# Performance work log

Hardware: AMD Instinct MI355X
Metric: run time of the kernel (lower is better)

Reference implementation:

```python
import jax, jax.numpy as jnp
import numpy as np

HIDDEN = 2048
HEAD_DIM = 128
GROUPS = 8
HEADS = HIDDEN // HEAD_DIM          # 16
HPG = HEADS // GROUPS               # heads per group = 2


def setup_inputs() -> dict:
    key = jax.random.key(0)
    ks = jax.random.split(key, 9)
    b, sl, sk = 2, 2048, 2048
    s = 0.02
    return {
        "q": jax.random.normal(ks[0], (b, sl, HIDDEN), jnp.float32),
        "k": jax.random.normal(ks[1], (b, sk, HIDDEN), jnp.float32),
        "v": jax.random.normal(ks[2], (b, sk, HIDDEN), jnp.float32),
        "Wq": jax.random.normal(ks[3], (HIDDEN, HIDDEN), jnp.float32) * s,
        "bq": jax.random.normal(ks[4], (HIDDEN,), jnp.float32) * s,
        "Wk": jax.random.normal(ks[5], (HIDDEN, HEAD_DIM * GROUPS), jnp.float32) * s,
        "bk": jax.random.normal(ks[6], (HEAD_DIM * GROUPS,), jnp.float32) * s,
        "Wv": jax.random.normal(ks[7], (HIDDEN, HEAD_DIM * GROUPS), jnp.float32) * s,
        "bv": jax.random.normal(ks[8], (HEAD_DIM * GROUPS,), jnp.float32) * s,
    }


def reference(q, k, v, Wq, bq, Wk, bk, Wv, bv):
    b, sl, _ = q.shape
    sk = k.shape[1]
    qp = q @ Wq + bq                                   # [b, sl, hidden]
    kp = k @ Wk + bk                                   # [b, sk, G*d]
    vp = v @ Wv + bv                                   # [b, sk, G*d]
    # head h = g*HPG + j uses group g, matching torch repeat_interleave on dim=1
    qh = qp.reshape(b, sl, GROUPS, HPG, HEAD_DIM).transpose(0, 2, 3, 1, 4)  # [b,G,hpg,sl,d]
    kh = kp.reshape(b, sk, GROUPS, HEAD_DIM).transpose(0, 2, 1, 3)          # [b,G,sk,d]
    vh = vp.reshape(b, sk, GROUPS, HEAD_DIM).transpose(0, 2, 1, 3)          # [b,G,sk,d]
    scale = 1.0 / jnp.sqrt(jnp.asarray(HEAD_DIM, qh.dtype))
    score = jnp.einsum("bghld,bgsd->bghls", qh, kh) * scale                 # [b,G,hpg,sl,sk]
    attn = jax.nn.softmax(score, axis=-1)
    out = jnp.einsum("bghls,bgsd->bghld", attn, vh)                         # [b,G,hpg,sl,d]
    out = out.transpose(0, 3, 1, 2, 4).reshape(b, sl, HIDDEN)
    return out
```

## Files before the change

kernel.cpp:

```cpp
#include <hip/hip_runtime.h>

typedef unsigned short u16;
typedef short v8s __attribute__((ext_vector_type(8)));
typedef float v4f __attribute__((ext_vector_type(4)));
typedef float v16f __attribute__((ext_vector_type(16)));

typedef __attribute__((address_space(3))) u16* lptr_t;
typedef const __attribute__((address_space(1))) void* gptr_t;

__device__ __forceinline__ u16 f2b(float f) {
  unsigned int u = __float_as_uint(f);
  u += 0x7fff + ((u >> 16) & 1);
  return (u16)(u >> 16);
}

__global__ __launch_bounds__(256) void prep_all(const float* __restrict__ q,
                                                const float* __restrict__ k,
                                                const float* __restrict__ v,
                                                const float* __restrict__ Wq,
                                                const float* __restrict__ Wk,
                                                const float* __restrict__ Wv,
                                                u16* __restrict__ qd,
                                                u16* __restrict__ kd,
                                                u16* __restrict__ vd,
                                                u16* __restrict__ wt) {
  __shared__ u16 tile[64][65];
  int blk = blockIdx.x;
  if (blk < 12288) {
    const float* s; u16* d;
    if (blk < 4096)      { s = q; d = qd; }
    else if (blk < 8192) { s = k; d = kd; blk -= 4096; }
    else                 { s = v; d = vd; blk -= 8192; }
    int i = (blk * 256 + threadIdx.x) * 8;
    float4 a = *(const float4*)&s[i];
    float4 b = *(const float4*)&s[i + 4];
    union { uint4 v4; u16 u[8]; } p;
    p.u[0] = f2b(a.x); p.u[1] = f2b(a.y); p.u[2] = f2b(a.z); p.u[3] = f2b(a.w);
    p.u[4] = f2b(b.x); p.u[5] = f2b(b.y); p.u[6] = f2b(b.z); p.u[7] = f2b(b.w);
    *(uint4*)&d[i] = p.v4;
    return;
  }
  blk -= 12288;
  const float* W; int N; u16* dst;
  if (blk < 1024)      { W = Wq; N = 2048; dst = wt; }
  else if (blk < 1536) { W = Wk; N = 1024; dst = wt + (size_t)2048 * 2048; blk -= 1024; }
  else                 { W = Wv; N = 1024; dst = wt + (size_t)3072 * 2048; blk -= 1536; }
  const int k0 = (blk & 31) * 64;
  const int n0 = (blk >> 5) * 64;
  const int t = threadIdx.x;
#pragma unroll
  for (int i = 0; i < 2; ++i) {
    int chunk = i * 256 + t;
    int kr = chunk >> 3;
    int nc = (chunk & 7) * 8;
    float4 a = *(const float4*)&W[(size_t)(k0 + kr) * N + n0 + nc];
    float4 b = *(const float4*)&W[(size_t)(k0 + kr) * N + n0 + nc + 4];
    tile[kr][nc + 0] = f2b(a.x); tile[kr][nc + 1] = f2b(a.y);
    tile[kr][nc + 2] = f2b(a.z); tile[kr][nc + 3] = f2b(a.w);
    tile[kr][nc + 4] = f2b(b.x); tile[kr][nc + 5] = f2b(b.y);
    tile[kr][nc + 6] = f2b(b.z); tile[kr][nc + 7] = f2b(b.w);
  }
  __syncthreads();
#pragma unroll
  for (int i = 0; i < 2; ++i) {
    int chunk = i * 256 + t;
    int nr = chunk >> 3;
    int kc = (chunk & 7) * 8;
    union { uint4 v; u16 u[8]; } cv;
#pragma unroll
    for (int j = 0; j < 8; ++j) cv.u[j] = tile[kc + j][nr];
    *(uint4*)&dst[(size_t)(n0 + nr) * 2048 + k0 + kc] = cv.v;
  }
}

__global__ __launch_bounds__(512, 2) void qkv_gemm8(const u16* __restrict__ qbf,
                                                    const u16* __restrict__ kbf,
                                                    const u16* __restrict__ vbf,
                                                    const u16* __restrict__ wt_all,
                                                    const float* __restrict__ bq,
                                                    const float* __restrict__ bk,
                                                    const float* __restrict__ bv,
                                                    u16* __restrict__ qp,
                                                    u16* __restrict__ kp,
                                                    u16* __restrict__ vpt) {
  __shared__ __align__(16) u16 A_sh[2][16384];
  __shared__ __align__(16) u16 B_sh[2][16384];

  const int bid = blockIdx.x;
  const int wg = (bid & 7) * 32 + (bid >> 3);
  const int m0 = (wg >> 4) * 256;
  const int n0 = (wg & 15) * 256;

  const int t = threadIdx.x;
  const int w = t >> 6, lane = t & 63;
  const int quad = lane >> 4, l16 = lane & 15;
  const int wr = w >> 2, wc = w & 3;

  const u16* Abase; const float* bias; int region, nloc0;
  if (n0 < 2048)      { Abase = qbf; bias = bq; region = 0; nloc0 = n0; }
  else if (n0 < 3072) { Abase = kbf; bias = bk; region = 1; nloc0 = n0 - 2048; }
  else                { Abase = vbf; bias = bv; region = 2; nloc0 = n0 - 3072; }

  const u16* GA = Abase + (size_t)m0 * 2048;
  const u16* GB = wt_all + (size_t)n0 * 2048;

  int offA[2][2], ldsA[2][2], offB[2][2], ldsB[2][2];
#pragma unroll
  for (int s_ = 0; s_ < 2; ++s_)
#pragma unroll
    for (int j = 0; j < 2; ++j) {
      int r0a = j * 128 + s_ * 64 + w * 8;
      int ra = r0a + (lane >> 3);
      offA[s_][j] = ra * 2048 + (((lane & 7) ^ (ra & 7)) << 3);
      ldsA[s_][j] = r0a * 64 + lane * 8;
      int r0b = j * 128 + s_ * 32 + (w >> 2) * 64 + (w & 3) * 8;
      int rb = r0b + (lane >> 3);
      offB[s_][j] = rb * 2048 + (((lane & 7) ^ (rb & 7)) << 3);
      ldsB[s_][j] = r0b * 64 + lane * 8;
    }

  int colR[2];
#pragma unroll
  for (int kk = 0; kk < 2; ++kk)
    colR[kk] = ((kk * 4 + quad) ^ (l16 & 7)) << 3;

#define ST_A(BUF, KEL, S_)                                                              \
  do {                                                                                  \
    _Pragma("unroll") for (int j_ = 0; j_ < 2; ++j_) {                                  \
      const u16* g_ = GA + (KEL) + offA[S_][j_];                                        \
      lptr_t l_ = (lptr_t)&A_sh[BUF][ldsA[S_][j_]];                                     \
      __builtin_amdgcn_global_load_lds((gptr_t)g_,                                      \
                                       (__attribute__((address_space(3))) void*)l_,     \
                                       16, 0, 0);                                       \
    }                                                                                   \
  } while (0)

#define ST_B(BUF, KEL, S_)                                                              \
  do {                                                                                  \
    _Pragma("unroll") for (int j_ = 0; j_ < 2; ++j_) {                                  \
      const u16* g_ = GB + (KEL) + offB[S_][j_];                                        \
      lptr_t l_ = (lptr_t)&B_sh[BUF][ldsB[S_][j_]];                                     \
      __builtin_amdgcn_global_load_lds((gptr_t)g_,                                      \
                                       (__attribute__((address_space(3))) void*)l_,     \
                                       16, 0, 0);                                       \
    }                                                                                   \
  } while (0)

#define RD_A(BUF, MS, DST)                                                              \
  do {                                                                                  \
    const int rb_ = wr * 128 + (MS) * 64;                                               \
    _Pragma("unroll") for (int m_ = 0; m_ < 4; ++m_)                                    \
    _Pragma("unroll") for (int kk_ = 0; kk_ < 2; ++kk_)                                 \
      DST[m_][kk_] = *(const v8s*)&A_sh[BUF][(rb_ + m_ * 16 + l16) * 64 + colR[kk_]];   \
  } while (0)

#define RD_B(BUF, NS)                                                                   \
  do {                                                                                  \
    const int rb_ = wc * 64 + (NS) * 32;                                                \
    _Pragma("unroll") for (int n_ = 0; n_ < 2; ++n_)                                    \
    _Pragma("unroll") for (int kk_ = 0; kk_ < 2; ++kk_)                                 \
      b[n_][kk_] = *(const v8s*)&B_sh[BUF][(rb_ + n_ * 16 + l16) * 64 + colR[kk_]];     \
  } while (0)

#define MM(AR, MS, NS)                                                                  \
  do {                                                                                  \
    __builtin_amdgcn_s_setprio(1);                                                      \
    _Pragma("unroll") for (int kk_ = 0; kk_ < 2; ++kk_)                                 \
    _Pragma("unroll") for (int m_ = 0; m_ < 4; ++m_)                                    \
    _Pragma("unroll") for (int n_ = 0; n_ < 2; ++n_)                                    \
      acc[(MS) * 4 + m_][(NS) * 2 + n_] = __builtin_amdgcn_mfma_f32_16x16x32_bf16(      \
          AR[m_][kk_], b[n_][kk_], acc[(MS) * 4 + m_][(NS) * 2 + n_], 0, 0, 0);         \
    __builtin_amdgcn_s_setprio(0);                                                      \
  } while (0)

#define PHASE_MID()                                                                     \
  do {                                                                                  \
    asm volatile("" ::: "memory");                                                      \
    __builtin_amdgcn_s_barrier();                                                       \
    asm volatile("s_waitcnt lgkmcnt(0)" ::: "memory");                                  \
    __builtin_amdgcn_sched_barrier(0);                                                  \
  } while (0)

#define PHASE_END()                                                                     \
  do {                                                                                  \
    asm volatile("" ::: "memory");                                                      \
    __builtin_amdgcn_s_barrier();                                                       \
    __builtin_amdgcn_sched_barrier(0);                                                  \
  } while (0)

#define PHASE_END_V()                                                                   \
  do {                                                                                  \
    asm volatile("s_waitcnt vmcnt(6)" ::: "memory");                                    \
    __builtin_amdgcn_s_barrier();                                                       \
    __builtin_amdgcn_sched_barrier(0);                                                  \
  } while (0)

  v4f acc[8][4] = {};
  v8s a0[4][2], a1[4][2], b[2][2];

  ST_A(0, 0, 0); ST_B(0, 0, 0); ST_A(0, 0, 1); ST_B(0, 0, 1);
  ST_B(1, 64, 0); ST_A(1, 64, 1); ST_B(1, 64, 1);
  asm volatile("s_waitcnt vmcnt(6)" ::: "memory");
  __builtin_amdgcn_s_barrier();
  __builtin_amdgcn_sched_barrier(0);

  for (int it = 0; it < 16; ++it) {
    const int k1 = (2 * it + 1) * 64;
    const int k2 = ((2 * it + 2) & 31) * 64;
    const int k3 = ((2 * it + 3) & 31) * 64;
    RD_A(0, 0, a0); RD_B(0, 0); ST_A(1, k1, 0); PHASE_MID(); MM(a0, 0, 0); PHASE_END();
    RD_A(0, 1, a1);             ST_B(0, k2, 0); PHASE_MID(); MM(a1, 1, 0); PHASE_END();
    RD_B(0, 1);                 ST_A(0, k2, 1); PHASE_MID(); MM(a1, 1, 1); PHASE_END();
                                ST_B(0, k2, 1); PHASE_MID(); MM(a0, 0, 1); PHASE_END_V();
    RD_A(1, 0, a0); RD_B(1, 0); ST_A(0, k2, 0); PHASE_MID(); MM(a0, 0, 0); PHASE_END();
    RD_A(1, 1, a1);             ST_B(1, k3, 0); PHASE_MID(); MM(a1, 1, 0); PHASE_END();
    RD_B(1, 1);                 ST_A(1, k3, 1); PHASE_MID(); MM(a1, 1, 1); PHASE_END();
                                ST_B(1, k3, 1); PHASE_MID(); MM(a0, 0, 1); PHASE_END_V();
  }

#undef ST_A
#undef ST_B
#undef RD_A
#undef RD_B
#undef MM
#undef PHASE_MID
#undef PHASE_END
#undef PHASE_END_V

#pragma unroll
  for (int n = 0; n < 4; ++n) {
    int nl = nloc0 + wc * 64 + n * 16 + l16;
    float bvl = bias[nl];
    if (region == 0) {
#pragma unroll
      for (int m = 0; m < 8; ++m)
#pragma unroll
        for (int r = 0; r < 4; ++r) {
          int mg = m0 + wr * 128 + m * 16 + quad * 4 + r;
          qp[(size_t)mg * 2048 + nl] = f2b((acc[m][n][r] + bvl) * 0.08838834764831845f);
        }
    } else if (region == 1) {
#pragma unroll
      for (int m = 0; m < 8; ++m)
#pragma unroll
        for (int r = 0; r < 4; ++r) {
          int mg = m0 + wr * 128 + m * 16 + quad * 4 + r;
          kp[(size_t)mg * 1024 + nl] = f2b(acc[m][n][r] + bvl);
        }
    } else {
      int g = nl >> 7, d = nl & 127;
#pragma unroll
      for (int m = 0; m < 8; ++m) {
        int mb = m0 + wr * 128 + m * 16 + quad * 4;
        int bb = mb >> 11, s = mb & 2047;
        ushort4 pk;
        pk.x = f2b(acc[m][n][0] + bvl);
        pk.y = f2b(acc[m][n][1] + bvl);
        pk.z = f2b(acc[m][n][2] + bvl);
        pk.w = f2b(acc[m][n][3] + bvl);
        *(ushort4*)&vpt[(((size_t)bb * 8 + g) * 128 + d) * 2048 + s] = pk;
      }
    }
  }
}

__global__ __launch_bounds__(256, 2) void gqa_attn2(const u16* __restrict__ qp,
                                                    const u16* __restrict__ kp,
                                                    const u16* __restrict__ vpt,
                                                    float* __restrict__ out) {
  __shared__ __align__(16) u16 K_sh[2][64 * 128];
  __shared__ __align__(16) u16 V_sh[2][128 * 64];

  const int qtile = blockIdx.x;
  const int head = blockIdx.y;
  const int batch = blockIdx.z;
  const int g = head >> 1;
  const int q0 = qtile * 128;

  const u16* qpb = qp + (size_t)batch * 2048 * 2048;
  const u16* kpb = kp + (size_t)batch * 2048 * 1024;
  const u16* vptb = vpt + (size_t)batch * 8 * 128 * 2048;
  float* outb = out + (size_t)batch * 2048 * 2048;

  const int t = threadIdx.x;
  const int wave = t >> 6, lane = t & 63;
  const int l = lane & 31, h = lane >> 5;

  v8s qf[8];
  {
    const u16* qrow = &qpb[(size_t)(q0 + wave * 32 + l) * 2048 + head * 128];
#pragma unroll
    for (int ks = 0; ks < 8; ++ks)
      qf[ks] = *(const v8s*)&qrow[ks * 16 + h * 8];
  }

  int colK[8];
#pragma unroll
  for (int ks = 0; ks < 8; ++ks) colK[ks] = ((2 * ks + h) ^ (l & 7)) * 8;

  int koff[4], voff[4];
#pragma unroll
  for (int i = 0; i < 4; ++i) {
    int krow = wave * 16 + i * 4 + (lane >> 4);
    int kg = (lane & 15) ^ (krow & 7);
    koff[i] = krow * 1024 + g * 128 + kg * 8;
    int vrow = wave * 32 + i * 8 + (lane >> 3);
    int vg = (lane & 7) ^ (vrow & 7);
    voff[i] = (g * 128 + vrow) * 2048 + vg * 8;
  }

#define STAGE_KV(BUF, S0)                                                               \
  do {                                                                                  \
    _Pragma("unroll") for (int i_ = 0; i_ < 4; ++i_) {                                  \
      const u16* gk_ = kpb + (size_t)(S0) * 1024 + koff[i_];                            \
      lptr_t lk_ = (lptr_t)&K_sh[BUF][(wave * 16 + i_ * 4) * 128] + lane * 8;           \
      __builtin_amdgcn_global_load_lds((gptr_t)gk_,                                     \
                                       (__attribute__((address_space(3))) void*)lk_,    \
                                       16, 0, 0);                                       \
      const u16* gv_ = vptb + voff[i_] + (S0);                                          \
      lptr_t lv_ = (lptr_t)&V_sh[BUF][(wave * 32 + i_ * 8) * 64] + lane * 8;            \
      __builtin_amdgcn_global_load_lds((gptr_t)gv_,                                     \
                                       (__attribute__((address_space(3))) void*)lv_,    \
                                       16, 0, 0);                                       \
    }                                                                                   \
  } while (0)

  v16f o_acc[4] = {};
  float rs = 0.0f;

  STAGE_KV(0, 0);
  __syncthreads();

  int cur = 0;
  for (int sc = 0; sc < 32; ++sc) {
    if (sc < 31) STAGE_KV(cur ^ 1, (sc + 1) * 64);

    v16f sacc[2] = {};
    __builtin_amdgcn_s_setprio(1);
#pragma unroll
    for (int kb = 0; kb < 2; ++kb)
#pragma unroll
      for (int ks = 0; ks < 8; ++ks) {
        v8s kf = *(const v8s*)&K_sh[cur][(kb * 32 + l) * 128 + colK[ks]];
        sacc[kb] = __builtin_amdgcn_mfma_f32_32x32x16_bf16(kf, qf[ks], sacc[kb], 0, 0, 0);
      }
    __builtin_amdgcn_s_setprio(0);

    unsigned int wv[16];
#pragma unroll
    for (int kb = 0; kb < 2; ++kb)
#pragma unroll
      for (int p = 0; p < 8; ++p) {
        float e0 = __expf(sacc[kb][2 * p]);
        float e1 = __expf(sacc[kb][2 * p + 1]);
        rs += e0 + e1;
        asm("v_cvt_pk_bf16_f32 %0, %1, %2" : "=v"(wv[kb * 8 + p]) : "v"(e0), "v"(e1));
      }

    v8s pa[4];
#pragma unroll
    for (int j = 0; j < 4; ++j) {
      unsigned int a = wv[j * 4 + 0], c = wv[j * 4 + 1];
      unsigned int b = wv[j * 4 + 2], d = wv[j * 4 + 3];
      asm("v_permlane32_swap_b32 %0, %1" : "+v"(a), "+v"(b));
      asm("v_permlane32_swap_b32 %0, %1" : "+v"(c), "+v"(d));
      union { unsigned int u[4]; v8s s; } pk;
      pk.u[0] = a; pk.u[1] = c; pk.u[2] = b; pk.u[3] = d;
      pa[j] = pk.s;
    }

    __builtin_amdgcn_s_setprio(1);
#pragma unroll
    for (int j = 0; j < 4; ++j)
#pragma unroll
      for (int db = 0; db < 4; ++db) {
        v8s vf = *(const v8s*)&V_sh[cur][(db * 32 + l) * 64 + colK[j]];
        o_acc[db] = __builtin_amdgcn_mfma_f32_32x32x16_bf16(pa[j], vf, o_acc[db], 0, 0, 0);
      }
    __builtin_amdgcn_s_setprio(0);

    __syncthreads();
    cur ^= 1;
  }

  float rst = rs + __shfl_xor(rs, 32, 64);
  float inv = 1.0f / rst;
#pragma unroll
  for (int r = 0; r < 16; ++r) {
    int qpat = (r & 3) + 8 * (r >> 2) + 4 * h;
    float invq = __shfl(inv, qpat, 64);
    int qrow = q0 + wave * 32 + qpat;
    float* orow = &outb[(size_t)qrow * 2048 + head * 128 + l];
#pragma unroll
    for (int db = 0; db < 4; ++db)
      orow[db * 32] = o_acc[db][r] * invq;
  }
#undef STAGE_KV
}

extern "C" void kernel_launch(void* const* d_in, const int* in_sizes, int n_in,
                              void* d_out, int out_size, void* d_ws, size_t ws_size,
                              hipStream_t stream) {
  const float* q  = (const float*)d_in[0];
  const float* k  = (const float*)d_in[1];
  const float* v  = (const float*)d_in[2];
  const float* Wq = (const float*)d_in[3];
  const float* bq = (const float*)d_in[4];
  const float* Wk = (const float*)d_in[5];
  const float* bk = (const float*)d_in[6];
  const float* Wv = (const float*)d_in[7];
  const float* bv = (const float*)d_in[8];
  float* out = (float*)d_out;
  char* ws = (char*)d_ws;

  u16* qbf    = (u16*)(ws + 0);
  u16* kbf    = (u16*)(ws + 16777216);
  u16* vbf    = (u16*)(ws + 33554432);
  u16* wt_all = (u16*)(ws + 50331648);
  u16* qp     = (u16*)(ws + 67108864);
  u16* kp     = (u16*)(ws + 83886080);
  u16* vpt    = (u16*)(ws + 92274688);

  prep_all<<<14336, 256, 0, stream>>>(q, k, v, Wq, Wk, Wv, qbf, kbf, vbf, wt_all);
  qkv_gemm8<<<256, 512, 0, stream>>>(qbf, kbf, vbf, wt_all,
                                     bq, bk, bv, qp, kp, vpt);
  gqa_attn2<<<dim3(16, 16, 2), 256, 0, stream>>>(qp, kp, vpt, out);
}
```

Before: 316.3 us.

## Load K/V directly from global into registers and use exp2 with prescaled Q

Removes the LDS double-buffered staging of K and V tiles and their barriers. Each wave instead reads its MFMA operand fragments directly from global memory. Folds log2(e) into the Q projection scale so softmax can use the hardware exp2 instruction. This trades shared-memory reuse and prefetch overlap for fewer synchronisations, at the risk of much higher global/L2 traffic and uncoalesced strided loads.

```diff
diff --git a/kernel.cpp b/kernel.cpp
--- a/kernel.cpp
+++ b/kernel.cpp
@@ -237,7 +237,7 @@
 #pragma unroll
         for (int r = 0; r < 4; ++r) {
           int mg = m0 + wr * 128 + m * 16 + quad * 4 + r;
-          qp[(size_t)mg * 2048 + nl] = f2b((acc[m][n][r] + bvl) * 0.08838834764831845f);
+          qp[(size_t)mg * 2048 + nl] = f2b((acc[m][n][r] + bvl) * 0.12751744518608807f);
         }
     } else if (region == 1) {
 #pragma unroll
@@ -264,13 +264,10 @@
   }
 }
 
-__global__ __launch_bounds__(256, 2) void gqa_attn2(const u16* __restrict__ qp,
+__global__ __launch_bounds__(256, 2) void gqa_attn3(const u16* __restrict__ qp,
                                                     const u16* __restrict__ kp,
                                                     const u16* __restrict__ vpt,
                                                     float* __restrict__ out) {
-  __shared__ __align__(16) u16 K_sh[2][64 * 128];
-  __shared__ __align__(16) u16 V_sh[2][128 * 64];
-
   const int qtile = blockIdx.x;
   const int head = blockIdx.y;
   const int batch = blockIdx.z;
@@ -294,56 +291,29 @@
       qf[ks] = *(const v8s*)&qrow[ks * 16 + h * 8];
   }
 
-  int colK[8];
-#pragma unroll
-  for (int ks = 0; ks < 8; ++ks) colK[ks] = ((2 * ks + h) ^ (l & 7)) * 8;
-
-  int koff[4], voff[4];
-#pragma unroll
-  for (int i = 0; i < 4; ++i) {
-    int krow = wave * 16 + i * 4 + (lane >> 4);
-    int kg = (lane & 15) ^ (krow & 7);
-    koff[i] = krow * 1024 + g * 128 + kg * 8;
-    int vrow = wave * 32 + i * 8 + (lane >> 3);
-    int vg = (lane & 7) ^ (vrow & 7);
-    voff[i] = (g * 128 + vrow) * 2048 + vg * 8;
-  }
-
-#define STAGE_KV(BUF, S0)                                                               \
-  do {                                                                                  \
-    _Pragma("unroll") for (int i_ = 0; i_ < 4; ++i_) {                                  \
-      const u16* gk_ = kpb + (size_t)(S0) * 1024 + koff[i_];                            \
-      lptr_t lk_ = (lptr_t)&K_sh[BUF][(wave * 16 + i_ * 4) * 128] + lane * 8;           \
-      __builtin_amdgcn_global_load_lds((gptr_t)gk_,                                     \
-                                       (__attribute__((address_space(3))) void*)lk_,    \
-                                       16, 0, 0);                                       \
-      const u16* gv_ = vptb + voff[i_] + (S0);                                          \
-      lptr_t lv_ = (lptr_t)&V_sh[BUF][(wave * 32 + i_ * 8) * 64] + lane * 8;            \
-      __builtin_amdgcn_global_load_lds((gptr_t)gv_,                                     \
-                                       (__attribute__((address_space(3))) void*)lv_,    \
-                                       16, 0, 0);                                       \
-    }                                                                                   \
-  } while (0)
+  const u16* Kbase = kpb + (size_t)l * 1024 + g * 128 + h * 8;
+  const u16* Vbase = vptb + ((size_t)g * 128 + l) * 2048 + h * 8;
 
   v16f o_acc[4] = {};
   float rs = 0.0f;
 
-  STAGE_KV(0, 0);
-  __syncthreads();
-
-  int cur = 0;
   for (int sc = 0; sc < 32; ++sc) {
-    if (sc < 31) STAGE_KV(cur ^ 1, (sc + 1) * 64);
+    const int s0 = sc * 64;
+
+    v8s kf[2][8];
+#pragma unroll
+    for (int kb = 0; kb < 2; ++kb)
+#pragma unroll
+      for (int ks = 0; ks < 8; ++ks)
+        kf[kb][ks] = *(const v8s*)&Kbase[(size_t)(s0 + kb * 32) * 1024 + ks * 16];
 
     v16f sacc[2] = {};
     __builtin_amdgcn_s_setprio(1);
 #pragma unroll
     for (int kb = 0; kb < 2; ++kb)
 #pragma unroll
-      for (int ks = 0; ks < 8; ++ks) {
-        v8s kf = *(const v8s*)&K_sh[cur][(kb * 32 + l) * 128 + colK[ks]];
-        sacc[kb] = __builtin_amdgcn_mfma_f32_32x32x16_bf16(kf, qf[ks], sacc[kb], 0, 0, 0);
-      }
+      for (int ks = 0; ks < 8; ++ks)
+        sacc[kb] = __builtin_amdgcn_mfma_f32_32x32x16_bf16(kf[kb][ks], qf[ks], sacc[kb], 0, 0, 0);
     __builtin_amdgcn_s_setprio(0);
 
     unsigned int wv[16];
@@ -351,8 +321,8 @@
     for (int kb = 0; kb < 2; ++kb)
 #pragma unroll
       for (int p = 0; p < 8; ++p) {
-        float e0 = __expf(sacc[kb][2 * p]);
-        float e1 = __expf(sacc[kb][2 * p + 1]);
+        float e0 = __builtin_amdgcn_exp2f(sacc[kb][2 * p]);
+        float e1 = __builtin_amdgcn_exp2f(sacc[kb][2 * p + 1]);
         rs += e0 + e1;
         asm("v_cvt_pk_bf16_f32 %0, %1, %2" : "=v"(wv[kb * 8 + p]) : "v"(e0), "v"(e1));
       }
@@ -374,13 +344,10 @@
     for (int j = 0; j < 4; ++j)
 #pragma unroll
       for (int db = 0; db < 4; ++db) {
-        v8s vf = *(const v8s*)&V_sh[cur][(db * 32 + l) * 64 + colK[j]];
+        v8s vf = *(const v8s*)&Vbase[(size_t)(db * 32) * 2048 + s0 + j * 16];
         o_acc[db] = __builtin_amdgcn_mfma_f32_32x32x16_bf16(pa[j], vf, o_acc[db], 0, 0, 0);
       }
     __builtin_amdgcn_s_setprio(0);
-
-    __syncthreads();
-    cur ^= 1;
   }
 
   float rst = rs + __shfl_xor(rs, 32, 64);
@@ -395,7 +362,6 @@
     for (int db = 0; db < 4; ++db)
       orow[db * 32] = o_acc[db][r] * invq;
   }
-#undef STAGE_KV
 }
 
 extern "C" void kernel_launch(void* const* d_in, const int* in_sizes, int n_in,
@@ -424,5 +390,5 @@
   prep_all<<<14336, 256, 0, stream>>>(q, k, v, Wq, Wk, Wv, qbf, kbf, vbf, wt_all);
   qkv_gemm8<<<256, 512, 0, stream>>>(qbf, kbf, vbf, wt_all,
                                      bq, bk, bv, qp, kp, vpt);
-  gqa_attn2<<<dim3(16, 16, 2), 256, 0, stream>>>(qp, kp, vpt, out);
-}
+  gqa_attn3<<<dim3(16, 16, 2), 256, 0, stream>>>(qp, kp, vpt, out);
+}
```

Result: slower. 476.0 us (+50.5%).
